# Performance work log

Hardware: AMD Instinct MI355X
Metric: run time of the kernel (lower is better)

The kernel has to match this reference:

```python
import jax, jax.numpy as jnp
import numpy as np

B, N1, N2, C2, K = 8, 2048, 128, 256, 3
D_POS, H0, H1 = 32, 512, 1024


def setup_inputs() -> dict:
    key = jax.random.key(0)
    ks = jax.random.split(key, 14)
    return {
        "xyz1": jax.random.normal(ks[0], (B, N1, 3), jnp.float32),
        "xyz2": jax.random.normal(ks[1], (B, N2, 3), jnp.float32),
        "feat2": jax.random.normal(ks[2], (B, N2, C2), jnp.float32),
        "lrf2": jax.random.normal(ks[3], (B, N2, 3, 3), jnp.float32),
        "w_pos": jax.random.normal(ks[4], (D_POS, 4), jnp.float32) * 0.1,
        "pos_scale": jax.random.uniform(ks[5], (D_POS,), jnp.float32, 0.5, 1.5),
        "pos_bias": jax.random.normal(ks[6], (D_POS,), jnp.float32) * 0.1,
        "w0": jax.random.normal(ks[7], (H0, C2 + D_POS), jnp.float32) * 0.05,
        "s0": jax.random.uniform(ks[8], (H0,), jnp.float32, 0.5, 1.5),
        "b0": jax.random.normal(ks[9], (H0,), jnp.float32) * 0.1,
        "w1": jax.random.normal(ks[10], (H1, H0), jnp.float32) * 0.04,
        "s1": jax.random.uniform(ks[11], (H1,), jnp.float32, 0.5, 1.5),
        "b1": jax.random.normal(ks[12], (H1,), jnp.float32) * 0.1,
        "k": K,
    }


def reference(xyz1, xyz2, feat2, lrf2, w_pos, pos_scale, pos_bias,
              w0, s0, b0, w1, s1, b1, k):
    Bb = xyz1.shape[0]
    # --- get_dists: full pairwise sqrt-distance matrix (B, N1, N2) ---
    d2 = (jnp.sum(xyz1 * xyz1, -1)[:, :, None]
          + jnp.sum(xyz2 * xyz2, -1)[:, None, :]
          - 2.0 * jnp.einsum('bmc,bnc->bmn', xyz1, xyz2))
    dists = jnp.sqrt(jnp.where(d2 < 0, 1e-7, d2))
    # --- k-NN: smallest k in ascending order (== torch.sort then slice) ---
    _, inds = jax.lax.top_k(-dists, k)                    # (B, N1, k)
    bidx = jnp.arange(Bb)[:, None, None]
    feat_nb = feat2[bidx, inds]                           # (B, N1, k, C2)
    close = xyz2[bidx, inds]                              # (B, N1, k, 3)
    lrf_nb = lrf2[bidx, inds]                             # (B, N1, k, 3, 3)
    # --- geometric angle embedding ---
    rel = xyz1[:, :, None, :] - close                     # (B, N1, k, 3)
    rel_norm = jnp.linalg.norm(rel, axis=-1)              # (B, N1, k)
    unit = rel / jnp.maximum(rel_norm, 1e-12)[..., None]  # F.normalize eps
    angle = jnp.einsum('bnkij,bnkj->bnki', lrf_nb, unit)  # (B, N1, k, 3)
    rp = jnp.concatenate([rel_norm[..., None], angle], -1)  # (B, N1, k, 4)
    # --- posembed: 1x1 Conv2d (no bias) + folded BN + LeakyReLU(0.2) ---
    pos = jax.nn.leaky_relu(
        jnp.einsum('bnkc,oc->bnko', rp, w_pos) * pos_scale + pos_bias, 0.2)
    # --- backbone: two 1x1 convs with folded BN + ReLU ---
    x = jnp.concatenate([feat_nb, pos], -1)               # (B, N1, k, C2+32)
    h0 = jax.nn.relu(jnp.einsum('bnkc,oc->bnko', x, w0) * s0 + b0)
    h1 = jax.nn.relu(jnp.einsum('bnkc,oc->bnko', h0, w1) * s1 + b1)
    # --- sum over neighbors, return (B, C_out, N1) like torch ---
    return jnp.transpose(jnp.sum(h1, axis=2), (0, 2, 1))
```

## Files before the change

### kernel.cpp

```cpp
#include <hip/hip_runtime.h>


typedef unsigned short u16;
typedef __bf16 bf16x8 __attribute__((ext_vector_type(8)));
typedef float f32x4 __attribute__((ext_vector_type(4)));
typedef u16 u16x4 __attribute__((ext_vector_type(4)));

#define BQ 8
#define N1Q 2048
#define N2Q 128
#define C2Q 256
#define DPOS 32
#define H0Q 512
#define H1Q 1024
#define NQ (BQ * N1Q)

#define WS_W0F 0u
#define WS_W0P 262144u
#define WS_W1 294912u
#define WS_F2B 1343488u
#define WS_F 1867776u
#define WS_H0 3964928u

__device__ __forceinline__ u16 f2bf(float f) {
  unsigned int u = __builtin_bit_cast(unsigned int, f);
  return (u16)((u + 0x7FFFu + ((u >> 16) & 1u)) >> 16);
}

__device__ __forceinline__ void load16_lds(const void* g, void* l) {
  __builtin_amdgcn_global_load_lds(
      (const __attribute__((address_space(1))) unsigned int*)g,
      (__attribute__((address_space(3))) unsigned int*)l, 16, 0, 0);
}

__global__ void convert_inputs(const float* __restrict__ w0,
                               const float* __restrict__ w1,
                               const float* __restrict__ feat2,
                               u16* __restrict__ w0f, u16* __restrict__ w0p,
                               u16* __restrict__ w1b, u16* __restrict__ f2b) {
  int i = blockIdx.x * 256 + threadIdx.x;
  if (i < 131072) {
    int h = i >> 8, c = i & 255;
    w0f[i] = f2bf(w0[h * 288 + c]);
  } else if (i < 147456) {
    int j = i - 131072;
    int h = j >> 5, c = j & 31;
    w0p[j] = f2bf(w0[h * 288 + 256 + c]);
  } else if (i < 671744) {
    int j = i - 147456;
    w1b[j] = f2bf(w1[j]);
  } else {
    int j = i - 671744;
    f2b[j] = f2bf(feat2[j]);
  }
}

__global__ __launch_bounds__(256, 2) void fgemm(const u16* __restrict__ A,
                                                const u16* __restrict__ W,
                                                float* __restrict__ F) {
  __shared__ alignas(16) u16 As[128 * 32];
  __shared__ alignas(16) u16 Bs[128 * 32];
  const int m0 = (blockIdx.x >> 2) * 128, n0 = (blockIdx.x & 3) * 128;
  const int t = threadIdx.x;
  const int wv = t >> 6, lane = t & 63;
  const int wm = wv >> 1, wn = wv & 1;
  const int quad = lane >> 4, cc = lane & 15;
  const int srow = lane & 15, skc = quad * 8;
  f32x4 acc[4][4] = {};

  for (int k0 = 0; k0 < 256; k0 += 32) {
#pragma unroll
    for (int i = 0; i < 2; i++) {
      int g = i * 4 + wv;
      load16_lds(A + (size_t)(m0 + g * 16 + srow) * 256 + k0 + skc,
                 (char*)As + g * 1024 + (lane << 4));
      load16_lds(W + (size_t)(n0 + g * 16 + srow) * 256 + k0 + skc,
                 (char*)Bs + g * 1024 + (lane << 4));
    }
    __syncthreads();
    bf16x8 af[4], bf[4];
#pragma unroll
    for (int mt = 0; mt < 4; mt++)
      af[mt] = *(const bf16x8*)((const char*)As + (wm * 4 + mt) * 1024 + (lane << 4));
#pragma unroll
    for (int nt = 0; nt < 4; nt++)
      bf[nt] = *(const bf16x8*)((const char*)Bs + (wn * 4 + nt) * 1024 + (lane << 4));
#pragma unroll
    for (int mt = 0; mt < 4; mt++)
#pragma unroll
      for (int nt = 0; nt < 4; nt++)
        acc[mt][nt] = __builtin_amdgcn_mfma_f32_16x16x32_bf16(
            af[mt], bf[nt], acc[mt][nt], 0, 0, 0);
    __syncthreads();
  }

#pragma unroll
  for (int nt = 0; nt < 4; nt++) {
    int gn = n0 + wn * 64 + nt * 16 + cc;
#pragma unroll
    for (int mt = 0; mt < 4; mt++) {
      int gm = m0 + wm * 64 + mt * 16 + quad * 4;
#pragma unroll
      for (int r = 0; r < 4; r++)
        F[(size_t)(gm + r) * H0Q + gn] = acc[mt][nt][r];
    }
  }
}

__global__ __launch_bounds__(256, 2) void build_h0(
    const float* __restrict__ xyz1, const float* __restrict__ xyz2,
    const float* __restrict__ lrf2, const float* __restrict__ w_pos,
    const float* __restrict__ pscale, const float* __restrict__ pbias,
    const u16* __restrict__ w0p, const float* __restrict__ F,
    const float* __restrict__ s0, const float* __restrict__ b0,
    u16* __restrict__ H0) {
  __shared__ float xyz2s[N2Q * 3];
  __shared__ float n2s[N2Q];
  __shared__ float lrfs[N2Q * 9];
  __shared__ float wps[DPOS * 4];
  __shared__ float pss[DPOS];
  __shared__ float pbs[DPOS];
  __shared__ int idxb[192];
  __shared__ float candd[64 * 13];
  __shared__ int candi[64 * 13];
  __shared__ alignas(16) u16 posb[12 * 512];

  const int t = threadIdx.x;
  const int qb = blockIdx.x * 64;
  const int b = qb >> 11;

  for (int i = t; i < N2Q * 3; i += 256) xyz2s[i] = xyz2[b * N2Q * 3 + i];
  for (int i = t; i < N2Q * 9; i += 256) lrfs[i] = lrf2[b * N2Q * 9 + i];
  if (t < DPOS * 4) wps[t] = w_pos[t];
  if (t < DPOS) { pss[t] = pscale[t]; pbs[t] = pbias[t]; }
  __syncthreads();
  if (t < N2Q) {
    float x = xyz2s[t * 3], y = xyz2s[t * 3 + 1], z = xyz2s[t * 3 + 2];
    n2s[t] = x * x + y * y + z * z;
  }
  __syncthreads();

  {
    const int ql = t >> 2, qt = t & 3;
    const int q = qb + ql;
    const float px = xyz1[q * 3], py = xyz1[q * 3 + 1], pz = xyz1[q * 3 + 2];
    const float pn = px * px + py * py + pz * pz;
    float d0 = 1e30f, d1 = 1e30f, d2v = 1e30f;
    int i0 = 0, i1 = 0, i2 = 0;
    const int ibeg = qt * 32;
    for (int i = ibeg; i < ibeg + 32; i++) {
      float dt = px * xyz2s[i * 3] + py * xyz2s[i * 3 + 1] + pz * xyz2s[i * 3 + 2];
      float d = pn + n2s[i] - 2.f * dt;
      if (d < d0) {
        d2v = d1; i2 = i1; d1 = d0; i1 = i0; d0 = d; i0 = i;
      } else if (d < d1) {
        d2v = d1; i2 = i1; d1 = d; i1 = i;
      } else if (d < d2v) {
        d2v = d; i2 = i;
      }
    }
    int base = ql * 13 + qt * 3;
    candd[base] = d0;      candi[base] = i0;
    candd[base + 1] = d1;  candi[base + 1] = i1;
    candd[base + 2] = d2v; candi[base + 2] = i2;
  }
  __syncthreads();

  if (t < 64) {
    float d0 = 1e30f, d1 = 1e30f, d2v = 1e30f;
    int i0 = 0, i1 = 0, i2 = 0;
    int base = t * 13;
#pragma unroll
    for (int c = 0; c < 12; c++) {
      float d = candd[base + c];
      int id = candi[base + c];
      if (d < d0) {
        d2v = d1; i2 = i1; d1 = d0; i1 = i0; d0 = d; i0 = id;
      } else if (d < d1) {
        d2v = d1; i2 = i1; d1 = d; i1 = id;
      } else if (d < d2v) {
        d2v = d; i2 = id;
      }
    }
    idxb[t] = i0;
    idxb[64 + t] = i1;
    idxb[128 + t] = i2;
  }
  __syncthreads();

  if (t < 192) {
    const int ql = t & 63;
    const int q = qb + ql;
    const float px = xyz1[q * 3], py = xyz1[q * 3 + 1], pz = xyz1[q * 3 + 2];
    const int id = idxb[t];
    float rx = px - xyz2s[id * 3];
    float ry = py - xyz2s[id * 3 + 1];
    float rz = pz - xyz2s[id * 3 + 2];
    float rn = sqrtf(rx * rx + ry * ry + rz * rz);
    float inv = 1.f / fmaxf(rn, 1e-12f);
    float ux = rx * inv, uy = ry * inv, uz = rz * inv;
    const float* L = lrfs + id * 9;
    float a0 = L[0] * ux + L[1] * uy + L[2] * uz;
    float a1 = L[3] * ux + L[4] * uy + L[5] * uz;
    float a2 = L[6] * ux + L[7] * uy + L[8] * uz;
    u16* pd = posb + (t >> 4) * 512 + (t & 15) * 8;
#pragma unroll
    for (int o = 0; o < DPOS; o++) {
      float v = wps[o * 4] * rn + wps[o * 4 + 1] * a0 + wps[o * 4 + 2] * a1 +
                wps[o * 4 + 3] * a2;
      v = v * pss[o] + pbs[o];
      v = (v >= 0.f) ? v : 0.2f * v;
      pd[(o >> 3) * 128 + (o & 7)] = f2bf(v);
    }
  }
  __syncthreads();

  const int wv = t >> 6, lane = t & 63;
  const int quad = lane >> 4, cc = lane & 15;
  const float* Fr[3];
  u16* Hr[3];
#pragma unroll
  for (int mt = 0; mt < 3; mt++) {
    int rl = wv * 48 + mt * 16 + cc;
    Fr[mt] = F + ((size_t)(b * N2Q + idxb[rl])) * H0Q;
    int jj = rl >> 6, ql = rl & 63;
    Hr[mt] = H0 + ((size_t)(jj * NQ) + qb + ql) * H0Q;
  }
  bf16x8 afr[3];
#pragma unroll
  for (int mt = 0; mt < 3; mt++)
    afr[mt] = *(const bf16x8*)((const char*)posb + (wv * 3 + mt) * 1024 + (lane << 4));
  const f32x4 zf = {};
  for (int n0 = 0; n0 < H0Q; n0 += 128) {
    bf16x8 bfr[8];
#pragma unroll
    for (int nt = 0; nt < 8; nt++)
      bfr[nt] = *(const bf16x8*)(w0p + (n0 + nt * 16 + cc) * 32 + quad * 8);
    f32x4 acc[3][8];
#pragma unroll
    for (int mt = 0; mt < 3; mt++)
#pragma unroll
      for (int nt = 0; nt < 8; nt++)
        acc[mt][nt] = __builtin_amdgcn_mfma_f32_16x16x32_bf16(bfr[nt], afr[mt],
                                                              zf, 0, 0, 0);
#pragma unroll
    for (int nt = 0; nt < 8; nt++) {
      int hb = n0 + nt * 16 + quad * 4;
      f32x4 sv = *(const f32x4*)(s0 + hb);
      f32x4 bvv = *(const f32x4*)(b0 + hb);
#pragma unroll
      for (int mt = 0; mt < 3; mt++) {
        f32x4 fv = *(const f32x4*)(Fr[mt] + hb);
        u16x4 o4;
#pragma unroll
        for (int r = 0; r < 4; r++) {
          float h = (fv[r] + acc[mt][nt][r]) * sv[r] + bvv[r];
          h = h > 0.f ? h : 0.f;
          o4[r] = f2bf(h);
        }
        *(u16x4*)(Hr[mt] + hb) = o4;
      }
    }
  }
}

__global__ __launch_bounds__(512, 2) void gemm2(const u16* __restrict__ A,
                                                const u16* __restrict__ W,
                                                const float* __restrict__ s,
                                                const float* __restrict__ bz,
                                                float* __restrict__ out) {
  __shared__ alignas(16) u16 As[3][128 * 32];
  __shared__ alignas(16) u16 Bs[3][128 * 32];
  const int id = blockIdx.x;
  const int xcd = id & 7, g = id >> 3;
  const int m0 = (xcd * 16 + (g >> 3)) * 128;
  const int n0 = (g & 7) * 128;
  const int t = threadIdx.x;
  const int wv = t >> 6, lane = t & 63;
  const int wm = wv >> 2, wn = wv & 3;
  const int quad = lane >> 4, cc = lane & 15;

  const int srow = lane & 15, skc = quad * 8;
  const size_t aOff = (size_t)(m0 + wv * 16 + srow) * 512 + skc;
  const size_t wOff = (size_t)(n0 + wv * 16 + srow) * 512 + skc;
  const int ldst = wv * 1024 + (lane << 4);

  float sv[2], bv[2];
#pragma unroll
  for (int nt = 0; nt < 2; nt++) {
    int gn = n0 + wn * 32 + nt * 16 + cc;
    sv[nt] = s[gn];
    bv[nt] = bz[gn];
  }

  auto stage = [&](int sIdx, int buf) {
    const u16* Aj = A + (size_t)(sIdx >> 4) * ((size_t)NQ * H0Q);
    const int k0 = (sIdx & 15) << 5;
    load16_lds(Aj + aOff + k0, (char*)As[buf] + ldst);
    load16_lds(W + wOff + (size_t)k0, (char*)Bs[buf] + ldst);
  };

  f32x4 sum[4][2] = {};
  f32x4 acc[4][2] = {};

  stage(0, 0);
  stage(1, 1);
  stage(2, 2);

#pragma unroll 3
  for (int sI = 0; sI < 48; sI++) {
    const int bi = sI % 3;
    asm volatile("s_waitcnt vmcnt(4)" ::: "memory");
    __builtin_amdgcn_s_barrier();
    bf16x8 af[4], bf[2];
#pragma unroll
    for (int mt = 0; mt < 4; mt++)
      af[mt] = *(const bf16x8*)((const char*)As[bi] + (wm * 4 + mt) * 1024 +
                                (lane << 4));
#pragma unroll
    for (int nt = 0; nt < 2; nt++)
      bf[nt] = *(const bf16x8*)((const char*)Bs[bi] + (wn * 2 + nt) * 1024 +
                                (lane << 4));
    asm volatile("s_waitcnt lgkmcnt(0)" ::: "memory");
    __builtin_amdgcn_s_barrier();
    if (sI + 3 < 48) stage(sI + 3, bi);
    __builtin_amdgcn_s_setprio(1);
#pragma unroll
    for (int mt = 0; mt < 4; mt++)
#pragma unroll
      for (int nt = 0; nt < 2; nt++)
        acc[mt][nt] = __builtin_amdgcn_mfma_f32_16x16x32_bf16(
            af[mt], bf[nt], acc[mt][nt], 0, 0, 0);
    __builtin_amdgcn_s_setprio(0);
    if ((sI & 15) == 15) {
#pragma unroll
      for (int mt = 0; mt < 4; mt++)
#pragma unroll
        for (int nt = 0; nt < 2; nt++) {
#pragma unroll
          for (int r = 0; r < 4; r++) {
            float h = acc[mt][nt][r] * sv[nt] + bv[nt];
            sum[mt][nt][r] += (h > 0.f ? h : 0.f);
          }
          acc[mt][nt] = f32x4{};
        }
    }
  }

#pragma unroll
  for (int nt = 0; nt < 2; nt++) {
    int gn = n0 + wn * 32 + nt * 16 + cc;
#pragma unroll
    for (int mt = 0; mt < 4; mt++) {
      int gm = m0 + wm * 64 + mt * 16 + quad * 4;
#pragma unroll
      for (int r = 0; r < 4; r++) {
        int q = gm + r;
        out[((size_t)(q >> 11) * H1Q + gn) * N1Q + (q & 2047)] = sum[mt][nt][r];
      }
    }
  }
}

extern "C" void kernel_launch(void* const* d_in, const int* in_sizes, int n_in,
                              void* d_out, int out_size, void* d_ws,
                              size_t ws_size, hipStream_t stream) {
  const float* xyz1 = (const float*)d_in[0];
  const float* xyz2 = (const float*)d_in[1];
  const float* feat2 = (const float*)d_in[2];
  const float* lrf2 = (const float*)d_in[3];
  const float* w_pos = (const float*)d_in[4];
  const float* pscale = (const float*)d_in[5];
  const float* pbias = (const float*)d_in[6];
  const float* w0 = (const float*)d_in[7];
  const float* s0 = (const float*)d_in[8];
  const float* b0 = (const float*)d_in[9];
  const float* w1 = (const float*)d_in[10];
  const float* s1 = (const float*)d_in[11];
  const float* b1 = (const float*)d_in[12];
  float* out = (float*)d_out;

  char* ws = (char*)d_ws;
  u16* w0f = (u16*)(ws + WS_W0F);
  u16* w0p = (u16*)(ws + WS_W0P);
  u16* w1b = (u16*)(ws + WS_W1);
  u16* f2b = (u16*)(ws + WS_F2B);
  float* F = (float*)(ws + WS_F);
  u16* H0 = (u16*)(ws + WS_H0);

  convert_inputs<<<933888 / 256, 256, 0, stream>>>(w0, w1, feat2, w0f, w0p,
                                                   w1b, f2b);
  fgemm<<<32, 256, 0, stream>>>(f2b, w0f, F);
  build_h0<<<NQ / 64, 256, 0, stream>>>(xyz1, xyz2, lrf2, w_pos, pscale,
                                        pbias, w0p, F, s0, b0, H0);
  gemm2<<<1024, 512, 0, stream>>>(H0, w1b, s1, b1, out);
}
```

Measured before the change: 242.1 us.

## Enlarge gemm2 tiles to 128x256 with BK=64 and peel pipeline tail

Changes the second GEMM's block tile from 128x128 to 128x256 and its K-step from 32 to 64. Each wave now computes a 64x64 output with 32 MFMAs per barrier pair, and the grid is halved to 512 blocks. The larger tile is meant to raise arithmetic intensity, cut W reloads and reduce barrier overhead per MFMA. In exchange it needs much more LDS (about 144KB for triple buffering) and more accumulator registers, which likely limits occupancy to one block per CU, and the tail is peeled with explicit vmcnt waits.

```diff
diff --git a/kernel.cpp b/kernel.cpp
--- a/kernel.cpp
+++ b/kernel.cpp
@@ -269,87 +269,113 @@
                                                 const float* __restrict__ s,
                                                 const float* __restrict__ bz,
                                                 float* __restrict__ out) {
-  __shared__ alignas(16) u16 As[3][128 * 32];
-  __shared__ alignas(16) u16 Bs[3][128 * 32];
+  __shared__ alignas(16) u16 As[3][128 * 64];
+  __shared__ alignas(16) u16 Bs[3][256 * 64];
   const int id = blockIdx.x;
   const int xcd = id & 7, g = id >> 3;
-  const int m0 = (xcd * 16 + (g >> 3)) * 128;
-  const int n0 = (g & 7) * 128;
+  const int m0 = (xcd * 16 + (g >> 2)) * 128;
+  const int n0 = (g & 3) * 256;
   const int t = threadIdx.x;
   const int wv = t >> 6, lane = t & 63;
   const int wm = wv >> 2, wn = wv & 3;
   const int quad = lane >> 4, cc = lane & 15;
-
-  const int srow = lane & 15, skc = quad * 8;
-  const size_t aOff = (size_t)(m0 + wv * 16 + srow) * 512 + skc;
-  const size_t wOff = (size_t)(n0 + wv * 16 + srow) * 512 + skc;
-  const int ldst = wv * 1024 + (lane << 4);
-
-  float sv[2], bv[2];
-#pragma unroll
-  for (int nt = 0; nt < 2; nt++) {
-    int gn = n0 + wn * 32 + nt * 16 + cc;
+  const int lr = lane & 15, lk = (lane >> 4) * 8;
+
+  const size_t aOff = (size_t)(m0 + wv * 16 + lr) * 512 + lk;
+  const size_t bOff = (size_t)(n0 + wv * 32 + lr) * 512 + lk;
+
+  float sv[4], bv[4];
+#pragma unroll
+  for (int nt = 0; nt < 4; nt++) {
+    int gn = n0 + wn * 64 + nt * 16 + cc;
     sv[nt] = s[gn];
     bv[nt] = bz[gn];
   }
 
-  auto stage = [&](int sIdx, int buf) {
-    const u16* Aj = A + (size_t)(sIdx >> 4) * ((size_t)NQ * H0Q);
-    const int k0 = (sIdx & 15) << 5;
-    load16_lds(Aj + aOff + k0, (char*)As[buf] + ldst);
-    load16_lds(W + wOff + (size_t)k0, (char*)Bs[buf] + ldst);
+  auto stage = [&](int kt, int bi) {
+    const u16* Ap = A + (size_t)(kt >> 3) * ((size_t)NQ * H0Q) + ((kt & 7) << 6);
+    const u16* Wp = W + ((kt & 7) << 6);
+    char* ab = (char*)As[bi] + (lane << 4);
+    char* bb = (char*)Bs[bi] + (lane << 4);
+    load16_lds(Ap + aOff, ab + wv * 1024);
+    load16_lds(Ap + aOff + 32, ab + (8 + wv) * 1024);
+    load16_lds(Wp + bOff, bb + (wv * 2) * 1024);
+    load16_lds(Wp + bOff + (size_t)16 * 512, bb + (wv * 2 + 1) * 1024);
+    load16_lds(Wp + bOff + 32, bb + (16 + wv * 2) * 1024);
+    load16_lds(Wp + bOff + (size_t)16 * 512 + 32, bb + (16 + wv * 2 + 1) * 1024);
   };
 
-  f32x4 sum[4][2] = {};
-  f32x4 acc[4][2] = {};
+  f32x4 sum[4][4] = {};
+  f32x4 acc[4][4] = {};
+
+  auto tile = [&](int bi, int ktStage) {
+    bf16x8 af[2][4], bf[2][4];
+    const char* ab = (const char*)As[bi] + (lane << 4);
+    const char* bb = (const char*)Bs[bi] + (lane << 4);
+#pragma unroll
+    for (int kk = 0; kk < 2; kk++)
+#pragma unroll
+      for (int mt = 0; mt < 4; mt++)
+        af[kk][mt] = *(const bf16x8*)(ab + (kk * 8 + wm * 4 + mt) * 1024);
+#pragma unroll
+    for (int kk = 0; kk < 2; kk++)
+#pragma unroll
+      for (int nt = 0; nt < 4; nt++)
+        bf[kk][nt] = *(const bf16x8*)(bb + (kk * 16 + wn * 4 + nt) * 1024);
+    asm volatile("s_waitcnt lgkmcnt(0)" ::: "memory");
+    __builtin_amdgcn_s_barrier();
+    if (ktStage >= 0) stage(ktStage, bi);
+    __builtin_amdgcn_s_setprio(1);
+#pragma unroll
+    for (int kk = 0; kk < 2; kk++)
+#pragma unroll
+      for (int mt = 0; mt < 4; mt++)
+#pragma unroll
+        for (int nt = 0; nt < 4; nt++)
+          acc[mt][nt] = __builtin_amdgcn_mfma_f32_16x16x32_bf16(
+              af[kk][mt], bf[kk][nt], acc[mt][nt], 0, 0, 0);
+    __builtin_amdgcn_s_setprio(0);
+  };
+
+  auto fold = [&]() {
+#pragma unroll
+    for (int mt = 0; mt < 4; mt++)
+#pragma unroll
+      for (int nt = 0; nt < 4; nt++) {
+#pragma unroll
+        for (int r = 0; r < 4; r++) {
+          float h = acc[mt][nt][r] * sv[nt] + bv[nt];
+          sum[mt][nt][r] += (h > 0.f ? h : 0.f);
+        }
+        acc[mt][nt] = f32x4{};
+      }
+  };
 
   stage(0, 0);
   stage(1, 1);
   stage(2, 2);
 
 #pragma unroll 3
-  for (int sI = 0; sI < 48; sI++) {
-    const int bi = sI % 3;
-    asm volatile("s_waitcnt vmcnt(4)" ::: "memory");
+  for (int kt = 0; kt < 21; kt++) {
+    asm volatile("s_waitcnt vmcnt(12)" ::: "memory");
     __builtin_amdgcn_s_barrier();
-    bf16x8 af[4], bf[2];
-#pragma unroll
-    for (int mt = 0; mt < 4; mt++)
-      af[mt] = *(const bf16x8*)((const char*)As[bi] + (wm * 4 + mt) * 1024 +
-                                (lane << 4));
-#pragma unroll
-    for (int nt = 0; nt < 2; nt++)
-      bf[nt] = *(const bf16x8*)((const char*)Bs[bi] + (wn * 2 + nt) * 1024 +
-                                (lane << 4));
-    asm volatile("s_waitcnt lgkmcnt(0)" ::: "memory");
-    __builtin_amdgcn_s_barrier();
-    if (sI + 3 < 48) stage(sI + 3, bi);
-    __builtin_amdgcn_s_setprio(1);
-#pragma unroll
-    for (int mt = 0; mt < 4; mt++)
-#pragma unroll
-      for (int nt = 0; nt < 2; nt++)
-        acc[mt][nt] = __builtin_amdgcn_mfma_f32_16x16x32_bf16(
-            af[mt], bf[nt], acc[mt][nt], 0, 0, 0);
-    __builtin_amdgcn_s_setprio(0);
-    if ((sI & 15) == 15) {
-#pragma unroll
-      for (int mt = 0; mt < 4; mt++)
-#pragma unroll
-        for (int nt = 0; nt < 2; nt++) {
-#pragma unroll
-          for (int r = 0; r < 4; r++) {
-            float h = acc[mt][nt][r] * sv[nt] + bv[nt];
-            sum[mt][nt][r] += (h > 0.f ? h : 0.f);
-          }
-          acc[mt][nt] = f32x4{};
-        }
-    }
-  }
-
-#pragma unroll
-  for (int nt = 0; nt < 2; nt++) {
-    int gn = n0 + wn * 32 + nt * 16 + cc;
+    tile(kt % 3, kt + 3);
+    if ((kt & 7) == 7) fold();
+  }
+  asm volatile("s_waitcnt vmcnt(12)" ::: "memory");
+  __builtin_amdgcn_s_barrier();
+  tile(0, -1);
+  asm volatile("s_waitcnt vmcnt(6)" ::: "memory");
+  __builtin_amdgcn_s_barrier();
+  tile(1, -1);
+  asm volatile("s_waitcnt vmcnt(0)" ::: "memory");
+  __builtin_amdgcn_s_barrier();
+  tile(2, -1);
+  fold();
+
+#pragma unroll
+  for (int nt = 0; nt < 4; nt++) {
+    int gn = n0 + wn * 64 + nt * 16 + cc;
 #pragma unroll
     for (int mt = 0; mt < 4; mt++) {
       int gm = m0 + wm * 64 + mt * 16 + quad * 4;
@@ -393,5 +419,5 @@
   fgemm<<<32, 256, 0, stream>>>(f2b, w0f, F);
   build_h0<<<NQ / 64, 256, 0, stream>>>(xyz1, xyz2, lrf2, w_pos, pscale,
                                         pbias, w0p, F, s0, b0, H0);
-  gemm2<<<1024, 512, 0, stream>>>(H0, w1b, s1, b1, out);
-}
+  gemm2<<<512, 512, 0, stream>>>(H0, w1b, s1, b1, out);
+}
```

Result: faster. 231.1 us (-4.5%).
